# Kernel optimization log

Measured on AMD Instinct MI355X. Metric: run time of the kernel, lower is better.

The kernel has to match this reference:

```python
import jax, jax.numpy as jnp
import numpy as np

B, T, H, NH = 2, 2048, 1024, 16
D = H // NH          # head dim = 64
K_CONV = 4           # short conv kernel size


def _dwconv_silu(x, w):
    # causal depthwise conv1d + silu; x:[B,T,C], w:[C,K]
    Kc = w.shape[1]
    xp = jnp.pad(x, ((0, 0), (Kc - 1, 0), (0, 0))).transpose(0, 2, 1)  # [B,C,T+K-1]
    y = jax.lax.conv_general_dilated(xp, w[:, None, :], (1,), 'VALID',
                                     feature_group_count=w.shape[0],
                                     dimension_numbers=('NCH', 'OIH', 'NCH'))
    return jax.nn.silu(y.transpose(0, 2, 1))


def _l2norm(x, eps=1e-6):
    return x * jax.lax.rsqrt(jnp.sum(x * x, -1, keepdims=True) + eps)


def _forward(hidden, Wq, Wk, Wv, conv_q, conv_k, conv_v, Wb, Wa, A_log, dt_bias, Wg, norm_w, Wo):
    Bh, Tt, Hh = hidden.shape
    nh = A_log.shape[0]
    d = Hh // nh
    q = _dwconv_silu(hidden @ Wq.T, conv_q).reshape(Bh, Tt, nh, d)
    k = _dwconv_silu(hidden @ Wk.T, conv_k).reshape(Bh, Tt, nh, d)
    v = _dwconv_silu(hidden @ Wv.T, conv_v).reshape(Bh, Tt, nh, d)
    q = _l2norm(q) * (d ** -0.5)
    k = _l2norm(k)
    beta = jax.nn.sigmoid(hidden @ Wb.T)                                  # [B,T,h]
    g = -jnp.exp(A_log) * jax.nn.softplus(hidden @ Wa.T + dt_bias)        # [B,T,h]

    def step(S, inp):
        qt, kt, vt, gt, bt = inp
        S = S * jnp.exp(gt)[..., None, None]                 # gated decay
        pred = jnp.einsum('bhk,bhkv->bhv', kt, S)            # current memory readout
        dv = (vt - pred) * bt[..., None]                     # delta-rule update
        S = S + jnp.einsum('bhk,bhv->bhkv', kt, dv)
        ot = jnp.einsum('bhk,bhkv->bhv', qt, S)
        return S, ot

    xs = (q.transpose(1, 0, 2, 3), k.transpose(1, 0, 2, 3), v.transpose(1, 0, 2, 3),
          g.transpose(1, 0, 2), beta.transpose(1, 0, 2))
    S0 = jnp.zeros((Bh, nh, d, d), hidden.dtype)
    _, o = jax.lax.scan(step, S0, xs)
    o = o.transpose(1, 0, 2, 3)                               # [B,T,h,d]
    gate = (hidden @ Wg.T).reshape(Bh, Tt, nh, d)
    o = o * jax.lax.rsqrt(jnp.mean(o * o, -1, keepdims=True) + 1e-5) * norm_w
    o = o * jax.nn.silu(gate)                                 # gated RMSNorm
    return o.reshape(Bh, Tt, Hh) @ Wo.T


def setup_inputs():
    key = jax.random.key(0)
    ks = jax.random.split(key, 16)
    s = 0.02
    return {
        'hidden': jax.random.normal(ks[0], (B, T, H), jnp.float32),
        'Wq': jax.random.normal(ks[1], (H, H), jnp.float32) * s,
        'Wk': jax.random.normal(ks[2], (H, H), jnp.float32) * s,
        'Wv': jax.random.normal(ks[3], (H, H), jnp.float32) * s,
        'conv_q': jax.random.normal(ks[4], (H, K_CONV), jnp.float32) * 0.5,
        'conv_k': jax.random.normal(ks[5], (H, K_CONV), jnp.float32) * 0.5,
        'conv_v': jax.random.normal(ks[6], (H, K_CONV), jnp.float32) * 0.5,
        'Wb': jax.random.normal(ks[7], (NH, H), jnp.float32) * s,
        'Wa': jax.random.normal(ks[8], (NH, H), jnp.float32) * s,
        'A_log': jnp.log(jax.random.uniform(ks[9], (NH,), jnp.float32, 1.0, 16.0)),
        'dt_bias': jnp.log(jnp.expm1(jax.random.uniform(ks[10], (NH,), jnp.float32, 1e-3, 0.1))),
        'Wg': jax.random.normal(ks[11], (H, H), jnp.float32) * s,
        'norm_w': jnp.ones((D,), jnp.float32),
        'Wo': jax.random.normal(ks[12], (H, H), jnp.float32) * s,
    }


def reference(hidden, Wq, Wk, Wv, conv_q, conv_k, conv_v, Wb, Wa, A_log, dt_bias, Wg, norm_w, Wo):
    return _forward(hidden, Wq, Wk, Wv, conv_q, conv_k, conv_v, Wb, Wa, A_log, dt_bias, Wg, norm_w, Wo)
```

## Files before the change

kernel.cpp:

```cpp
#include <hip/hip_runtime.h>
#include <hip/hip_bf16.h>

typedef unsigned short u16;
typedef __attribute__((ext_vector_type(4))) float f32x4;
typedef __attribute__((ext_vector_type(8))) short bf16x8;

#define TLEN 2048
#define NHEAD 16
#define HD 1024

__device__ inline u16 f2bf(float f) {
  unsigned x = __float_as_uint(f);
  return (u16)((x + 0x7fffu + ((x >> 16) & 1u)) >> 16);
}
__device__ inline float bf2f(u16 u) { return __uint_as_float(((unsigned)u) << 16); }

__device__ inline void storev(float* p, float v) { *p = v; }
__device__ inline void storev(u16* p, float v)   { *p = f2bf(v); }

__device__ inline int swz(int row, int col) {
  return (row << 7) + ((((col >> 3) ^ (row & 7)) << 4)) + ((col & 7) << 1);
}
__device__ inline bf16x8 frag(const u16* base, int row, int kslot) {
  return *(const bf16x8*)((const char*)base + (row << 7) +
                          (((kslot ^ (row & 7)) << 4)));
}

__global__ __launch_bounds__(256) void cvt_all(
    const float* __restrict__ h,  const float* __restrict__ wq,
    const float* __restrict__ wk, const float* __restrict__ wv,
    const float* __restrict__ wg, const float* __restrict__ wo,
    const float* __restrict__ Wb, const float* __restrict__ Wa,
    u16* __restrict__ dh,  u16* __restrict__ dhlo,
    u16* __restrict__ dwq, u16* __restrict__ dwk,
    u16* __restrict__ dwv, u16* __restrict__ dwg, u16* __restrict__ dwo,
    u16* __restrict__ dwba_h, u16* __restrict__ dwba_l) {
  const int b = blockIdx.x;
  if (b < 4096) {
    const size_t i = (size_t)b * 256 + threadIdx.x;
    float4 v = *(const float4*)(h + i * 4);
    ushort4 hi, lo;
    hi.x = f2bf(v.x); lo.x = f2bf(v.x - bf2f(hi.x));
    hi.y = f2bf(v.y); lo.y = f2bf(v.y - bf2f(hi.y));
    hi.z = f2bf(v.z); lo.z = f2bf(v.z - bf2f(hi.z));
    hi.w = f2bf(v.w); lo.w = f2bf(v.w - bf2f(hi.w));
    *(ushort4*)(dh + i * 4) = hi;
    *(ushort4*)(dhlo + i * 4) = lo;
  } else if (b < 9216) {
    const int wsel = (b - 4096) >> 10;
    const size_t i = (size_t)((b - 4096) & 1023) * 256 + threadIdx.x;
    const float* s; u16* d;
    switch (wsel) {
      case 0: s = wq; d = dwq; break;
      case 1: s = wk; d = dwk; break;
      case 2: s = wv; d = dwv; break;
      case 3: s = wg; d = dwg; break;
      default: s = wo; d = dwo; break;
    }
    float4 v = *(const float4*)(s + i * 4);
    ushort4 u;
    u.x = f2bf(v.x); u.y = f2bf(v.y); u.z = f2bf(v.z); u.w = f2bf(v.w);
    *(ushort4*)(d + i * 4) = u;
  } else {
    const size_t i = (size_t)(b - 9216) * 256 + threadIdx.x;
    const size_t flat = i * 4;
    const float* src = (flat < 16384) ? (Wb + flat) : (Wa + (flat - 16384));
    float4 v = *(const float4*)src;
    ushort4 hi, lo;
    hi.x = f2bf(v.x); lo.x = f2bf(v.x - bf2f(hi.x));
    hi.y = f2bf(v.y); lo.y = f2bf(v.y - bf2f(hi.y));
    hi.z = f2bf(v.z); lo.z = f2bf(v.z - bf2f(hi.z));
    hi.w = f2bf(v.w); lo.w = f2bf(v.w - bf2f(hi.w));
    *(ushort4*)(dwba_h + flat) = hi;
    *(ushort4*)(dwba_l + flat) = lo;
  }
}

__global__ __launch_bounds__(256, 2) void gemm_big(
    const u16* __restrict__ A,
    const u16* __restrict__ W0p, const u16* __restrict__ W1p,
    const u16* __restrict__ W2p, const u16* __restrict__ W3p,
    u16* __restrict__ C0, u16* __restrict__ C1,
    u16* __restrict__ C2, u16* __restrict__ C3,
    int M, int N, int K) {
  const u16* W; u16* C;
  switch (blockIdx.z) {
    case 0: W = W0p; C = C0; break;
    case 1: W = W1p; C = C1; break;
    case 2: W = W2p; C = C2; break;
    default: W = W3p; C = C3; break;
  }
  const int tid = threadIdx.x;
  const int lane = tid & 63, wid = tid >> 6;
  const int fr = lane & 15, fq = lane >> 4;
  const int row0 = blockIdx.y * 256, col0 = blockIdx.x * 128;
  __shared__ __align__(16) u16 As[256 * 64];
  __shared__ __align__(16) u16 Bs[128 * 64];

  const u16* aSrc[8]; const u16* bSrc[4];
#pragma unroll
  for (int it = 0; it < 8; ++it) {
    const int s = it * 256 + tid;
    const int r = s >> 3, cc = s & 7;
    aSrc[it] = A + (size_t)(row0 + r) * K + (cc ^ (r & 7)) * 8;
  }
#pragma unroll
  for (int it = 0; it < 4; ++it) {
    const int s = it * 256 + tid;
    const int r = s >> 3, cc = s & 7;
    bSrc[it] = W + (size_t)(col0 + r) * K + (cc ^ (r & 7)) * 8;
  }
  int aOff[4][2], bOff[8][2];
#pragma unroll
  for (int m = 0; m < 4; ++m)
#pragma unroll
    for (int kk = 0; kk < 2; ++kk) {
      const int ra = wid * 64 + m * 16 + fr;
      aOff[m][kk] = ra * 128 + ((((kk << 2) | fq) ^ (ra & 7)) << 4);
    }
#pragma unroll
  for (int n = 0; n < 8; ++n)
#pragma unroll
    for (int kk = 0; kk < 2; ++kk) {
      const int rb = n * 16 + fr;
      bOff[n][kk] = rb * 128 + ((((kk << 2) | fq) ^ (rb & 7)) << 4);
    }

  f32x4 acc[4][8] = {};
  for (int k0 = 0; k0 < K; k0 += 64) {
#pragma unroll
    for (int it = 0; it < 8; ++it)
      __builtin_amdgcn_global_load_lds(
          (const __attribute__((address_space(1))) void*)(aSrc[it] + k0),
          (__attribute__((address_space(3))) void*)((char*)As + (it * 256 + tid) * 16),
          16, 0, 0);
#pragma unroll
    for (int it = 0; it < 4; ++it)
      __builtin_amdgcn_global_load_lds(
          (const __attribute__((address_space(1))) void*)(bSrc[it] + k0),
          (__attribute__((address_space(3))) void*)((char*)Bs + (it * 256 + tid) * 16),
          16, 0, 0);
    __syncthreads();
#pragma unroll
    for (int kk = 0; kk < 2; ++kk) {
      bf16x8 af[4], bfr[8];
#pragma unroll
      for (int m = 0; m < 4; ++m)
        af[m] = *(const bf16x8*)((const char*)As + aOff[m][kk]);
#pragma unroll
      for (int n = 0; n < 8; ++n)
        bfr[n] = *(const bf16x8*)((const char*)Bs + bOff[n][kk]);
#pragma unroll
      for (int m = 0; m < 4; ++m)
#pragma unroll
        for (int n = 0; n < 8; ++n)
          acc[m][n] = __builtin_amdgcn_mfma_f32_16x16x32_bf16(af[m], bfr[n], acc[m][n], 0, 0, 0);
    }
    __syncthreads();
  }
#pragma unroll
  for (int m = 0; m < 4; ++m)
#pragma unroll
    for (int n = 0; n < 8; ++n)
#pragma unroll
      for (int r = 0; r < 4; ++r) {
        const int gr = row0 + wid * 64 + m * 16 + fq * 4 + r;
        const int gc = col0 + n * 16 + fr;
        C[(size_t)gr * N + gc] = f2bf(acc[m][n][r]);
      }
}

template <typename OutT, int MT>
__global__ __launch_bounds__(256) void gemm_lin(
    const u16* __restrict__ A, const u16* __restrict__ W,
    OutT* __restrict__ C, int M, int N, int K) {
  const int tid = threadIdx.x;
  const int lane = tid & 63, wid = tid >> 6;
  const int wr = wid >> 1, wc = wid & 1;
  const int fr = lane & 15, fq = lane >> 4;
  const int row0 = blockIdx.y * (MT * 32), col0 = blockIdx.x * 128;
  __shared__ __align__(16) u16 As[MT * 32 * 64];
  __shared__ __align__(16) u16 Bs[128 * 64];

  const u16* aSrc[MT]; const u16* bSrc[4];
#pragma unroll
  for (int it = 0; it < MT; ++it) {
    const int c = it * 256 + tid;
    const int r = c >> 3, cc = c & 7, sc = cc ^ (r & 7);
    aSrc[it] = A + (size_t)(row0 + r) * K + sc * 8;
  }
#pragma unroll
  for (int it = 0; it < 4; ++it) {
    const int c = it * 256 + tid;
    const int r = c >> 3, cc = c & 7, sc = cc ^ (r & 7);
    bSrc[it] = W + (size_t)(col0 + r) * K + sc * 8;
  }
  int aOff[MT][2], bOff[4][2];
#pragma unroll
  for (int m = 0; m < MT; ++m)
#pragma unroll
    for (int kk = 0; kk < 2; ++kk) {
      const int ra = wr * (MT * 16) + m * 16 + fr;
      aOff[m][kk] = ra * 128 + ((((kk << 2) | fq) ^ (fr & 7)) << 4);
    }
#pragma unroll
  for (int n = 0; n < 4; ++n)
#pragma unroll
    for (int kk = 0; kk < 2; ++kk) {
      const int rb = wc * 64 + n * 16 + fr;
      bOff[n][kk] = rb * 128 + ((((kk << 2) | fq) ^ (fr & 7)) << 4);
    }

  f32x4 acc[MT][4] = {};
  for (int k0 = 0; k0 < K; k0 += 64) {
#pragma unroll
    for (int it = 0; it < MT; ++it)
      __builtin_amdgcn_global_load_lds(
          (const __attribute__((address_space(1))) void*)(aSrc[it] + k0),
          (__attribute__((address_space(3))) void*)((char*)As + (it * 256 + wid * 64) * 16),
          16, 0, 0);
#pragma unroll
    for (int it = 0; it < 4; ++it)
      __builtin_amdgcn_global_load_lds(
          (const __attribute__((address_space(1))) void*)(bSrc[it] + k0),
          (__attribute__((address_space(3))) void*)((char*)Bs + (it * 256 + wid * 64) * 16),
          16, 0, 0);
    __syncthreads();
#pragma unroll
    for (int kk = 0; kk < 2; ++kk) {
      bf16x8 af[MT], bfr[4];
#pragma unroll
      for (int m = 0; m < MT; ++m)
        af[m] = *(const bf16x8*)((const char*)As + aOff[m][kk]);
#pragma unroll
      for (int n = 0; n < 4; ++n)
        bfr[n] = *(const bf16x8*)((const char*)Bs + bOff[n][kk]);
#pragma unroll
      for (int m = 0; m < MT; ++m)
#pragma unroll
        for (int n = 0; n < 4; ++n)
          acc[m][n] = __builtin_amdgcn_mfma_f32_16x16x32_bf16(af[m], bfr[n], acc[m][n], 0, 0, 0);
    }
    __syncthreads();
  }
#pragma unroll
  for (int m = 0; m < MT; ++m)
#pragma unroll
    for (int n = 0; n < 4; ++n)
#pragma unroll
      for (int r = 0; r < 4; ++r) {
        const int gr = row0 + wr * (MT * 16) + m * 16 + fq * 4 + r;
        const int gc = col0 + wc * 64 + n * 16 + fr;
        storev(&C[(size_t)gr * N + gc], acc[m][n][r]);
      }
}

__global__ __launch_bounds__(256) void small_mfma(
    const u16* __restrict__ hhi, const u16* __restrict__ hlo,
    const u16* __restrict__ whi, const u16* __restrict__ wlo,
    const float* __restrict__ A_log, const float* __restrict__ dtb,
    float* __restrict__ bbuf, float* __restrict__ gbuf) {
  extern __shared__ char smc[];
  u16* Ahi = (u16*)smc;
  u16* Alo = (u16*)(smc + 32768);
  float* Red = (float*)(smc + 65536);
  const int tid = threadIdx.x;
  const int row0 = blockIdx.x * 16;
#pragma unroll
  for (int i = 0; i < 8; ++i) {
    const int slot = tid + 256 * i;
    const int r = slot >> 7, s = slot & 127;
    const int ss = s ^ (r & 7);
    const size_t src = (size_t)(row0 + r) * 1024 + (size_t)ss * 8;
    __builtin_amdgcn_global_load_lds(
        (const __attribute__((address_space(1))) void*)(hhi + src),
        (__attribute__((address_space(3))) void*)(Ahi + (size_t)slot * 8), 16, 0, 0);
    __builtin_amdgcn_global_load_lds(
        (const __attribute__((address_space(1))) void*)(hlo + src),
        (__attribute__((address_space(3))) void*)(Alo + (size_t)slot * 8), 16, 0, 0);
  }
  __syncthreads();
  const int w = tid >> 6, lane = tid & 63, fr = lane & 15, fq = lane >> 4;
  f32x4 acc[2] = {};
#pragma unroll
  for (int kk = 0; kk < 8; ++kk) {
    const int s = w * 32 + kk * 4 + fq;
    const size_t k = (size_t)w * 256 + kk * 32 + fq * 8;
    const int aoff = ((fr << 7) + (s ^ (fr & 7))) * 8;
    bf16x8 ah = *(const bf16x8*)(Ahi + aoff);
    bf16x8 al = *(const bf16x8*)(Alo + aoff);
#pragma unroll
    for (int ct = 0; ct < 2; ++ct) {
      const size_t boff = (size_t)(ct * 16 + fr) * 1024 + k;
      bf16x8 bh = *(const bf16x8*)(whi + boff);
      bf16x8 bl = *(const bf16x8*)(wlo + boff);
      acc[ct] = __builtin_amdgcn_mfma_f32_16x16x32_bf16(ah, bh, acc[ct], 0, 0, 0);
      acc[ct] = __builtin_amdgcn_mfma_f32_16x16x32_bf16(ah, bl, acc[ct], 0, 0, 0);
      acc[ct] = __builtin_amdgcn_mfma_f32_16x16x32_bf16(al, bh, acc[ct], 0, 0, 0);
    }
  }
#pragma unroll
  for (int ct = 0; ct < 2; ++ct)
#pragma unroll
    for (int rr = 0; rr < 4; ++rr)
      Red[(w * 16 + fq * 4 + rr) * 33 + ct * 16 + fr] = acc[ct][rr];
  __syncthreads();
  if (tid < 128) {
    const int row = tid >> 3, cg = (tid & 7) * 4;
#pragma unroll
    for (int j = 0; j < 4; ++j) {
      const int col = cg + j;
      const float s = Red[(0 * 16 + row) * 33 + col] + Red[(1 * 16 + row) * 33 + col]
                    + Red[(2 * 16 + row) * 33 + col] + Red[(3 * 16 + row) * 33 + col];
      const int grow = row0 + row;
      if (col < 16) {
        bbuf[grow * NHEAD + col] = 1.f / (1.f + __expf(-s));
      } else {
        const int hh = col - 16;
        const float xs = s + dtb[hh];
        const float sp = (xs > 20.f) ? xs : log1pf(__expf(xs));
        gbuf[grow * NHEAD + hh] = -__expf(A_log[hh]) * sp;
      }
    }
  }
}

__global__ __launch_bounds__(256) void chunk_local(
    const u16* __restrict__ qp, const u16* __restrict__ kp, const u16* __restrict__ vp,
    const float* __restrict__ cq, const float* __restrict__ ck, const float* __restrict__ cv,
    const float* __restrict__ gbuf, const float* __restrict__ bbuf,
    u16* __restrict__ Phi, u16* __restrict__ Plo, u16* __restrict__ Ug,
    u16* __restrict__ Rg, u16* __restrict__ Yg) {
  __shared__ __align__(16) u16 Kb[64 * 64];
  __shared__ __align__(16) u16 Qb[64 * 64];
  __shared__ __align__(16) u16 K2T[64 * 64];
  __shared__ __align__(16) u16 KWt[64 * 64];
  __shared__ __align__(16) u16 Vt[64 * 64];
  __shared__ __align__(16) u16 Zb[64 * 64];
  __shared__ __align__(16) u16 Zt[64 * 64];
  __shared__ __align__(16) u16 Mb[64 * 72];
  __shared__ __align__(16) float Cb[16 * 64];
  __shared__ float bcs[64], bet[64], e2v[64], Bv[64];
  u16* WTh = Mb;
  u16* uTh = KWt;
  u16* Gb  = Vt;

  const int bid = blockIdx.x;
  const int c = bid & 31, bh = bid >> 5;
  const int b = bh >> 4, h = bh & 15;
  const int tid = threadIdx.x;

  {
    int* zp = (int*)Zt;
#pragma unroll
    for (int i = 0; i < 8; ++i) zp[tid + 256 * i] = 0;
  }
  if (tid < 64) {
    const size_t gi = (size_t)((b * TLEN + c * 64) + tid) * NHEAD + h;
    bet[tid] = bbuf[gi];
    float v = gbuf[gi];
#pragma unroll
    for (int ofs = 1; ofs < 64; ofs <<= 1) {
      float tt = __shfl_up(v, ofs);
      if (tid >= ofs) v += tt;
    }
    bcs[tid] = v;
  }
  __syncthreads();
  if (tid < 64) {
    const float blast = bcs[63];
    Bv[tid]  = __expf(bcs[tid]);
    e2v[tid] = __expf(blast - bcs[tid]);
  }
  __syncthreads();

  {
    const int dq = (tid & 15) * 4;
    const int col = h * 64 + dq;
    float4 wq4[4], wk4[4], wv4[4];
#pragma unroll
    for (int jj = 0; jj < 4; ++jj) {
      wq4[jj] = *(const float4*)(cq + (size_t)(col + jj) * 4);
      wk4[jj] = *(const float4*)(ck + (size_t)(col + jj) * 4);
      wv4[jj] = *(const float4*)(cv + (size_t)(col + jj) * 4);
    }
#pragma unroll
    for (int i = 0; i < 4; ++i) {
      const int r = i * 16 + (tid >> 4);
      const int tcur = c * 64 + r;
      ushort4 xq[4], xk[4], xv[4];
#pragma unroll
      for (int m = 0; m < 4; ++m) {
        const int tt = tcur - 3 + m;
        if (tt >= 0) {
          const size_t a = (size_t)(b * TLEN + tt) * HD + col;
          xq[m] = *(const ushort4*)(qp + a);
          xk[m] = *(const ushort4*)(kp + a);
          xv[m] = *(const ushort4*)(vp + a);
        } else {
          xq[m] = ushort4{0, 0, 0, 0}; xk[m] = xq[m]; xv[m] = xq[m];
        }
      }
      float yq[4], yk[4], yv[4];
      float ssq = 0.f, ssk = 0.f;
#pragma unroll
      for (int jj = 0; jj < 4; ++jj) {
        float aq = wq4[jj].x * bf2f(((const u16*)&xq[0])[jj]) +
                   wq4[jj].y * bf2f(((const u16*)&xq[1])[jj]) +
                   wq4[jj].z * bf2f(((const u16*)&xq[2])[jj]) +
                   wq4[jj].w * bf2f(((const u16*)&xq[3])[jj]);
        float ak = wk4[jj].x * bf2f(((const u16*)&xk[0])[jj]) +
                   wk4[jj].y * bf2f(((const u16*)&xk[1])[jj]) +
                   wk4[jj].z * bf2f(((const u16*)&xk[2])[jj]) +
                   wk4[jj].w * bf2f(((const u16*)&xk[3])[jj]);
        float av = wv4[jj].x * bf2f(((const u16*)&xv[0])[jj]) +
                   wv4[jj].y * bf2f(((const u16*)&xv[1])[jj]) +
                   wv4[jj].z * bf2f(((const u16*)&xv[2])[jj]) +
                   wv4[jj].w * bf2f(((const u16*)&xv[3])[jj]);
        yq[jj] = aq / (1.f + __expf(-aq));
        yk[jj] = ak / (1.f + __expf(-ak));
        yv[jj] = av / (1.f + __expf(-av));
        ssq += yq[jj] * yq[jj];
        ssk += yk[jj] * yk[jj];
      }
      ssq += __shfl_xor(ssq, 1); ssq += __shfl_xor(ssq, 2);
      ssq += __shfl_xor(ssq, 4); ssq += __shfl_xor(ssq, 8);
      ssk += __shfl_xor(ssk, 1); ssk += __shfl_xor(ssk, 2);
      ssk += __shfl_xor(ssk, 4); ssk += __shfl_xor(ssk, 8);
      const float qsc = rsqrtf(ssq + 1e-6f) * 0.125f;
      const float ksc = rsqrtf(ssk + 1e-6f);
      const float bR = bet[r], e2R = e2v[r], wscR = bR * Bv[r];
      ushort4 qo, ko;
      float kvf[4];
#pragma unroll
      for (int jj = 0; jj < 4; ++jj) kvf[jj] = yk[jj] * ksc;
      qo.x = f2bf(yq[0] * qsc); qo.y = f2bf(yq[1] * qsc);
      qo.z = f2bf(yq[2] * qsc); qo.w = f2bf(yq[3] * qsc);
      ko.x = f2bf(kvf[0]); ko.y = f2bf(kvf[1]);
      ko.z = f2bf(kvf[2]); ko.w = f2bf(kvf[3]);
      *(ushort4*)((char*)Qb + swz(r, dq)) = qo;
      *(ushort4*)((char*)Kb + swz(r, dq)) = ko;
#pragma unroll
      for (int jj = 0; jj < 4; ++jj) {
        *(u16*)((char*)K2T + swz(dq + jj, r)) = f2bf(kvf[jj] * e2R);
        *(u16*)((char*)KWt + swz(dq + jj, r)) = f2bf(kvf[jj] * wscR);
        *(u16*)((char*)Vt  + swz(dq + jj, r)) = f2bf(yv[jj] * bR);
      }
    }
  }
  __syncthreads();

  const int w = tid >> 6, lane = tid & 63, fr = lane & 15, fq = lane >> 4;
  {
    bf16x8 ka0 = frag(Kb, w * 16 + fr, fq);
    bf16x8 ka1 = frag(Kb, w * 16 + fr, 4 + fq);
#pragma unroll
    for (int tc = 0; tc < 4; ++tc) {
      bf16x8 kb0 = frag(Kb, tc * 16 + fr, fq);
      bf16x8 kb1 = frag(Kb, tc * 16 + fr, 4 + fq);
      f32x4 a = {};
      a = __builtin_amdgcn_mfma_f32_16x16x32_bf16(ka0, kb0, a, 0, 0, 0);
      a = __builtin_amdgcn_mfma_f32_16x16x32_bf16(ka1, kb1, a, 0, 0, 0);
#pragma unroll
      for (int rr = 0; rr < 4; ++rr) {
        const int t = w * 16 + fq * 4 + rr, s = tc * 16 + fr;
        const float mv = (s < t) ? bet[t] * __expf(bcs[t] - bcs[s]) * a[rr] : 0.f;
        Mb[t * 72 + s] = f2bf(mv);
      }
    }
  }
  __syncthreads();

#pragma unroll 1
  for (int bi = 0; bi < 4; ++bi) {
    {
      const char* mrow = (const char*)Mb + (size_t)(bi * 16 + fr) * 144;
      bf16x8 ma0 = *(const bf16x8*)(mrow + fq * 16);
      bf16x8 ma1 = *(const bf16x8*)(mrow + 64 + fq * 16);
      bf16x8 zt0 = frag(Zt, w * 16 + fr, fq);
      bf16x8 zt1 = frag(Zt, w * 16 + fr, 4 + fq);
      f32x4 a = {};
      a = __builtin_amdgcn_mfma_f32_16x16x32_bf16(ma0, zt0, a, 0, 0, 0);
      a = __builtin_amdgcn_mfma_f32_16x16x32_bf16(ma1, zt1, a, 0, 0, 0);
#pragma unroll
      for (int rr = 0; rr < 4; ++rr)
        Cb[(fq * 4 + rr) * 64 + w * 16 + fr] = a[rr];
    }
    __syncthreads();
    if (tid < 64) {
      const int j = tid;
      float z[16];
#pragma unroll
      for (int t = 0; t < 16; ++t) {
        float acc = ((bi * 16 + t) == j ? 1.f : 0.f) - Cb[t * 64 + j];
        const u16* mrow = Mb + (size_t)(bi * 16 + t) * 72 + bi * 16;
#pragma unroll
        for (int s = 0; s < t; ++s) acc -= bf2f(mrow[s]) * z[s];
        z[t] = acc;
      }
#pragma unroll
      for (int t = 0; t < 16; ++t)
        *(u16*)((char*)Zb + swz(bi * 16 + t, j)) = f2bf(z[t]);
#pragma unroll
      for (int t4 = 0; t4 < 4; ++t4) {
        ushort4 zz;
        zz.x = f2bf(z[t4 * 4 + 0]); zz.y = f2bf(z[t4 * 4 + 1]);
        zz.z = f2bf(z[t4 * 4 + 2]); zz.w = f2bf(z[t4 * 4 + 3]);
        *(ushort4*)((char*)Zt + swz(j, bi * 16 + t4 * 4)) = zz;
      }
    }
    __syncthreads();
  }

  f32x4 accW[4], accu[4], accG[4];
  {
    bf16x8 kw0 = frag(KWt, w * 16 + fr, fq), kw1 = frag(KWt, w * 16 + fr, 4 + fq);
    bf16x8 vt0 = frag(Vt,  w * 16 + fr, fq), vt1 = frag(Vt,  w * 16 + fr, 4 + fq);
    bf16x8 qa0 = frag(Qb,  w * 16 + fr, fq), qa1 = frag(Qb,  w * 16 + fr, 4 + fq);
#pragma unroll
    for (int tc = 0; tc < 4; ++tc) {
      bf16x8 z0 = frag(Zb, tc * 16 + fr, fq), z1 = frag(Zb, tc * 16 + fr, 4 + fq);
      bf16x8 kb0 = frag(Kb, tc * 16 + fr, fq), kb1 = frag(Kb, tc * 16 + fr, 4 + fq);
      f32x4 aw = {}, au = {}, ag = {};
      aw = __builtin_amdgcn_mfma_f32_16x16x32_bf16(kw0, z0, aw, 0, 0, 0);
      aw = __builtin_amdgcn_mfma_f32_16x16x32_bf16(kw1, z1, aw, 0, 0, 0);
      au = __builtin_amdgcn_mfma_f32_16x16x32_bf16(vt0, z0, au, 0, 0, 0);
      au = __builtin_amdgcn_mfma_f32_16x16x32_bf16(vt1, z1, au, 0, 0, 0);
      ag = __builtin_amdgcn_mfma_f32_16x16x32_bf16(qa0, kb0, ag, 0, 0, 0);
      ag = __builtin_amdgcn_mfma_f32_16x16x32_bf16(qa1, kb1, ag, 0, 0, 0);
      accW[tc] = aw; accu[tc] = au; accG[tc] = ag;
    }
  }
  __syncthreads();
#pragma unroll
  for (int tc = 0; tc < 4; ++tc)
#pragma unroll
    for (int rr = 0; rr < 4; ++rr) {
      const int ro = w * 16 + fq * 4 + rr, co = tc * 16 + fr;
      *(u16*)((char*)WTh + swz(ro, co)) = f2bf(accW[tc][rr]);
      *(u16*)((char*)uTh + swz(ro, co)) = f2bf(accu[tc][rr]);
      const float gv = (co <= ro) ? accG[tc][rr] * __expf(bcs[ro] - bcs[co]) : 0.f;
      *(u16*)((char*)Gb + swz(ro, co)) = f2bf(gv);
    }
  __syncthreads();

  {
    bf16x8 k20 = frag(K2T, w * 16 + fr, fq), k21 = frag(K2T, w * 16 + fr, 4 + fq);
    bf16x8 g0  = frag(Gb,  w * 16 + fr, fq), g1  = frag(Gb,  w * 16 + fr, 4 + fq);
    const float bl = Bv[63];
    const size_t off = (size_t)bid * 4096;
#pragma unroll
    for (int tc = 0; tc < 4; ++tc) {
      bf16x8 w0 = frag(WTh, tc * 16 + fr, fq), w1 = frag(WTh, tc * 16 + fr, 4 + fq);
      bf16x8 u0 = frag(uTh, tc * 16 + fr, fq), u1 = frag(uTh, tc * 16 + fr, 4 + fq);
      f32x4 aP = {}, aU = {}, aR = {}, aY = {};
      aP = __builtin_amdgcn_mfma_f32_16x16x32_bf16(k20, w0, aP, 0, 0, 0);
      aP = __builtin_amdgcn_mfma_f32_16x16x32_bf16(k21, w1, aP, 0, 0, 0);
      aU = __builtin_amdgcn_mfma_f32_16x16x32_bf16(k20, u0, aU, 0, 0, 0);
      aU = __builtin_amdgcn_mfma_f32_16x16x32_bf16(k21, u1, aU, 0, 0, 0);
      aR = __builtin_amdgcn_mfma_f32_16x16x32_bf16(g0, w0, aR, 0, 0, 0);
      aR = __builtin_amdgcn_mfma_f32_16x16x32_bf16(g1, w1, aR, 0, 0, 0);
      aY = __builtin_amdgcn_mfma_f32_16x16x32_bf16(g0, u0, aY, 0, 0, 0);
      aY = __builtin_amdgcn_mfma_f32_16x16x32_bf16(g1, u1, aY, 0, 0, 0);
#pragma unroll
      for (int rr = 0; rr < 4; ++rr) {
        const int ar = w * 16 + fq * 4 + rr, cb = tc * 16 + fr;
        const float pv = ((ar == cb) ? bl : 0.f) - aP[rr];
        const u16 phv = f2bf(pv);
        Phi[off + ar * 64 + cb] = phv;
        Plo[off + ar * 64 + cb] = f2bf(pv - bf2f(phv));
        Ug[off + ar * 64 + cb] = f2bf(aU[rr]);
        const float qv = bf2f(*(const u16*)((const char*)Qb + swz(ar, cb)));
        Rg[off + ar * 64 + cb] = f2bf(Bv[ar] * qv - aR[rr]);
        Yg[off + ar * 64 + cb] = f2bf(aY[rr]);
      }
    }
  }
}

__global__ __launch_bounds__(256) void state_step(
    const u16* __restrict__ Phi, const u16* __restrict__ Plo,
    const u16* __restrict__ Ug, u16* __restrict__ Sst) {
  __shared__ __align__(16) u16 Sth[2][64 * 64];
  __shared__ __align__(16) u16 Stl[2][64 * 64];
  const int bh = blockIdx.x;
  const int tid = threadIdx.x;
  const int w = tid >> 6, lane = tid & 63, fr = lane & 15, fq = lane >> 4;
  const size_t bbase = (size_t)bh * 32 * 4096;
  {
    int* p0 = (int*)&Sth[0][0];
    int* p1 = (int*)&Stl[0][0];
#pragma unroll
    for (int i = 0; i < 8; ++i) { p0[tid + 256 * i] = 0; p1[tid + 256 * i] = 0; }
    const ushort4 z4 = {0, 0, 0, 0};
#pragma unroll
    for (int i = 0; i < 4; ++i)
      *(ushort4*)(Sst + bbase + (size_t)tid * 16 + i * 4) = z4;
  }
  bf16x8 ph[2], pl[2];
  float uin[4][4];
#pragma unroll
  for (int kk = 0; kk < 2; ++kk) {
    const size_t ao = bbase + (size_t)(w * 16 + fr) * 64 + (kk * 4 + fq) * 8;
    ph[kk] = *(const bf16x8*)(Phi + ao);
    pl[kk] = *(const bf16x8*)(Plo + ao);
  }
#pragma unroll
  for (int tc = 0; tc < 4; ++tc)
#pragma unroll
    for (int rr = 0; rr < 4; ++rr)
      uin[tc][rr] = bf2f(Ug[bbase + (size_t)(w * 16 + fq * 4 + rr) * 64 + tc * 16 + fr]);
  __syncthreads();
  int cur = 0;
  for (int c = 0; c < 32; ++c) {
    f32x4 acc[4];
    bf16x8 phc[2] = {ph[0], ph[1]}, plc[2] = {pl[0], pl[1]};
#pragma unroll
    for (int tc = 0; tc < 4; ++tc)
#pragma unroll
      for (int rr = 0; rr < 4; ++rr) acc[tc][rr] = uin[tc][rr];
    if (c + 1 < 32) {
      const size_t off = bbase + (size_t)(c + 1) * 4096;
#pragma unroll
      for (int kk = 0; kk < 2; ++kk) {
        const size_t ao = off + (size_t)(w * 16 + fr) * 64 + (kk * 4 + fq) * 8;
        ph[kk] = *(const bf16x8*)(Phi + ao);
        pl[kk] = *(const bf16x8*)(Plo + ao);
      }
#pragma unroll
      for (int tc = 0; tc < 4; ++tc)
#pragma unroll
        for (int rr = 0; rr < 4; ++rr)
          uin[tc][rr] = bf2f(Ug[off + (size_t)(w * 16 + fq * 4 + rr) * 64 + tc * 16 + fr]);
    }
#pragma unroll
    for (int tc = 0; tc < 4; ++tc) {
#pragma unroll
      for (int kk = 0; kk < 2; ++kk) {
        bf16x8 sh = frag(&Sth[cur][0], tc * 16 + fr, kk * 4 + fq);
        bf16x8 sl = frag(&Stl[cur][0], tc * 16 + fr, kk * 4 + fq);
        acc[tc] = __builtin_amdgcn_mfma_f32_16x16x32_bf16(phc[kk], sh, acc[tc], 0, 0, 0);
        acc[tc] = __builtin_amdgcn_mfma_f32_16x16x32_bf16(phc[kk], sl, acc[tc], 0, 0, 0);
        acc[tc] = __builtin_amdgcn_mfma_f32_16x16x32_bf16(plc[kk], sh, acc[tc], 0, 0, 0);
      }
    }
    const int nxt = cur ^ 1;
    const size_t offn = bbase + (size_t)(c + 1) * 4096;
#pragma unroll
    for (int tc = 0; tc < 4; ++tc)
#pragma unroll
      for (int rr = 0; rr < 4; ++rr) {
        const float v = acc[tc][rr];
        const int row = w * 16 + fq * 4 + rr;
        const int col = tc * 16 + fr;
        const u16 hv = f2bf(v);
        *(u16*)((char*)&Sth[nxt][0] + swz(col, row)) = hv;
        *(u16*)((char*)&Stl[nxt][0] + swz(col, row)) = f2bf(v - bf2f(hv));
        if (c + 1 < 32) Sst[offn + (size_t)row * 64 + col] = hv;
      }
    cur = nxt;
    __syncthreads();
  }
}

__global__ __launch_bounds__(256) void chunk_out(
    const u16* __restrict__ Rg, const u16* __restrict__ Yg,
    const u16* __restrict__ Sst, const u16* __restrict__ gatep,
    const float* __restrict__ norm_w, u16* __restrict__ outb) {
  __shared__ float Rs[64 * 65];
  __shared__ float Ss[64 * 65];
  const int bid = blockIdx.x;
  const int c = bid & 31, bh = bid >> 5, b = bh >> 4, h = bh & 15;
  const int tid = threadIdx.x;
  const size_t off = (size_t)bid * 4096;
#pragma unroll
  for (int i = 0; i < 2; ++i) {
    const int idx = i * 2048 + tid * 8;
    const int row = idx >> 6, col = idx & 63;
    const ushort4 r0 = *(const ushort4*)(Rg + off + idx);
    const ushort4 r1 = *(const ushort4*)(Rg + off + idx + 4);
    const ushort4 s0 = *(const ushort4*)(Sst + off + idx);
    const ushort4 s1 = *(const ushort4*)(Sst + off + idx + 4);
    float* rd = &Rs[row * 65 + col];
    rd[0]=bf2f(r0.x); rd[1]=bf2f(r0.y); rd[2]=bf2f(r0.z); rd[3]=bf2f(r0.w);
    rd[4]=bf2f(r1.x); rd[5]=bf2f(r1.y); rd[6]=bf2f(r1.z); rd[7]=bf2f(r1.w);
    float* sd = &Ss[row * 65 + col];
    sd[0]=bf2f(s0.x); sd[1]=bf2f(s0.y); sd[2]=bf2f(s0.z); sd[3]=bf2f(s0.w);
    sd[4]=bf2f(s1.x); sd[5]=bf2f(s1.y); sd[6]=bf2f(s1.z); sd[7]=bf2f(s1.w);
  }
  __syncthreads();
  const int tr = tid >> 4, tc = tid & 15;
  float acc[4][4];
#pragma unroll
  for (int i = 0; i < 4; ++i) {
    const ushort4 y = *(const ushort4*)(Yg + off + (4*tr+i)*64 + 4*tc);
    acc[i][0] = bf2f(y.x); acc[i][1] = bf2f(y.y);
    acc[i][2] = bf2f(y.z); acc[i][3] = bf2f(y.w);
  }
  for (int k = 0; k < 64; ++k) {
    float r0 = Rs[(4*tr+0)*65+k], r1 = Rs[(4*tr+1)*65+k],
          r2 = Rs[(4*tr+2)*65+k], r3 = Rs[(4*tr+3)*65+k];
    float s0 = Ss[k*65+4*tc+0], s1 = Ss[k*65+4*tc+1],
          s2 = Ss[k*65+4*tc+2], s3 = Ss[k*65+4*tc+3];
    acc[0][0]+=r0*s0; acc[0][1]+=r0*s1; acc[0][2]+=r0*s2; acc[0][3]+=r0*s3;
    acc[1][0]+=r1*s0; acc[1][1]+=r1*s1; acc[1][2]+=r1*s2; acc[1][3]+=r1*s3;
    acc[2][0]+=r2*s0; acc[2][1]+=r2*s1; acc[2][2]+=r2*s2; acc[2][3]+=r2*s3;
    acc[3][0]+=r3*s0; acc[3][1]+=r3*s1; acc[3][2]+=r3*s2; acc[3][3]+=r3*s3;
  }
  const float4 nw4 = *(const float4*)(norm_w + 4 * tc);
  const size_t btbase = (size_t)(b * TLEN + c * 64);
#pragma unroll
  for (int i = 0; i < 4; ++i) {
    float rs = acc[i][0]*acc[i][0] + acc[i][1]*acc[i][1]
             + acc[i][2]*acc[i][2] + acc[i][3]*acc[i][3];
    rs += __shfl_xor(rs, 1); rs += __shfl_xor(rs, 2);
    rs += __shfl_xor(rs, 4); rs += __shfl_xor(rs, 8);
    const float inv = rsqrtf(rs * (1.0f / 64.0f) + 1e-5f);
    const int t = 4 * tr + i;
    const size_t goff = (btbase + t) * 1024 + h * 64 + 4 * tc;
    const ushort4 gv = *(const ushort4*)(gatep + goff);
    const float g0 = bf2f(gv.x), g1 = bf2f(gv.y), g2 = bf2f(gv.z), g3 = bf2f(gv.w);
    ushort4 ov;
    ov.x = f2bf(acc[i][0] * inv * nw4.x * (g0 / (1.f + __expf(-g0))));
    ov.y = f2bf(acc[i][1] * inv * nw4.y * (g1 / (1.f + __expf(-g1))));
    ov.z = f2bf(acc[i][2] * inv * nw4.z * (g2 / (1.f + __expf(-g2))));
    ov.w = f2bf(acc[i][3] * inv * nw4.w * (g3 / (1.f + __expf(-g3))));
    *(ushort4*)(outb + goff) = ov;
  }
}

extern "C" void kernel_launch(void* const* d_in, const int* in_sizes, int n_in,
                              void* d_out, int out_size, void* d_ws, size_t ws_size,
                              hipStream_t stream) {
  const float* hidden = (const float*)d_in[0];
  const float* Wq     = (const float*)d_in[1];
  const float* Wk     = (const float*)d_in[2];
  const float* Wv     = (const float*)d_in[3];
  const float* cq     = (const float*)d_in[4];
  const float* ck     = (const float*)d_in[5];
  const float* cv     = (const float*)d_in[6];
  const float* Wb     = (const float*)d_in[7];
  const float* Wa     = (const float*)d_in[8];
  const float* A_log  = (const float*)d_in[9];
  const float* dtb    = (const float*)d_in[10];
  const float* Wg     = (const float*)d_in[11];
  const float* nw     = (const float*)d_in[12];
  const float* Wo     = (const float*)d_in[13];

  char* p = (char*)d_ws;
  const size_t MB = 1u << 20;
  u16* h_bf = (u16*)(p + 0 * MB);
  u16* wq_b = (u16*)(p + 8 * MB);
  u16* wk_b = (u16*)(p + 10 * MB);
  u16* wv_b = (u16*)(p + 12 * MB);
  u16* wg_b = (u16*)(p + 14 * MB);
  u16* Phi = (u16*)(p + 0 * MB);
  u16* Plo = (u16*)(p + 8 * MB);
  u16* wo_b = (u16*)(p + 16 * MB);
  u16* qp_b = (u16*)(p + 18 * MB);
  u16* kp_b = (u16*)(p + 26 * MB);
  u16* vp_b = (u16*)(p + 34 * MB);
  u16* gp_b = (u16*)(p + 42 * MB);
  u16*   of_b = vp_b;
  float* gbuf = (float*)(p + 50 * MB);
  float* bbuf = (float*)(p + 50 * MB + 262144);
  u16* Ug  = (u16*)(p + 51 * MB);
  u16* Rg  = (u16*)(p + 59 * MB);
  u16* Yg  = (u16*)(p + 67 * MB);
  u16* Sst = (u16*)(p + 75 * MB);
  u16* hlo_b = (u16*)(p + 83 * MB);
  u16* wba_h = (u16*)(p + 91 * MB);
  u16* wba_l = (u16*)(p + 91 * MB + 65536);

  cvt_all<<<9248, 256, 0, stream>>>(hidden, Wq, Wk, Wv, Wg, Wo, Wb, Wa,
                                    h_bf, hlo_b, wq_b, wk_b, wv_b, wg_b, wo_b,
                                    wba_h, wba_l);

  gemm_big<<<dim3(8, 16, 4), 256, 0, stream>>>(
      h_bf, wq_b, wk_b, wv_b, wg_b, qp_b, kp_b, vp_b, gp_b, 4096, 1024, 1024);

  const int sm_lds = 65536 + 8448;
  hipFuncSetAttribute((const void*)small_mfma,
                      hipFuncAttributeMaxDynamicSharedMemorySize, sm_lds);
  small_mfma<<<256, 256, sm_lds, stream>>>(h_bf, hlo_b, wba_h, wba_l,
                                           A_log, dtb, bbuf, gbuf);

  chunk_local<<<1024, 256, 0, stream>>>(qp_b, kp_b, vp_b, cq, ck, cv,
                                        gbuf, bbuf, Phi, Plo, Ug, Rg, Yg);
  state_step<<<32, 256, 0, stream>>>(Phi, Plo, Ug, Sst);
  chunk_out<<<1024, 256, 0, stream>>>(Rg, Yg, Sst, gp_b, nw, of_b);

  gemm_lin<float, 2><<<dim3(8, 64, 1), 256, 0, stream>>>(
      of_b, wo_b, (float*)d_out, 4096, 1024, 1024);
}
```

Baseline: 181.4 us.

## Use MFMA in chunk_out, packed bf16 conversions, and a revised LDS swizzle

Several unrelated changes. chunk_out drops its fp32 LDS FMA loop and instead runs bf16 MFMA straight from global memory, reading a transposed stored state that the scan kernel now writes with vector stores. Float-to-bf16 rounding throughout now uses the packed v_cvt_pk_bf16_f32 instruction. The LDS swizzle XOR pattern now mixes in higher row bits to cut bank conflicts. The rounding path changes from the manual routine to the hardware conversion, which may differ slightly on NaN or edge values.

```diff
diff --git a/kernel.cpp b/kernel.cpp
--- a/kernel.cpp
+++ b/kernel.cpp
@@ -15,15 +15,22 @@
 }
 __device__ inline float bf2f(u16 u) { return __uint_as_float(((unsigned)u) << 16); }
 
+__device__ inline unsigned pkbf(float lo, float hi) {
+  unsigned r;
+  asm("v_cvt_pk_bf16_f32 %0, %1, %2" : "=v"(r) : "v"(lo), "v"(hi));
+  return r;
+}
+
 __device__ inline void storev(float* p, float v) { *p = v; }
 __device__ inline void storev(u16* p, float v)   { *p = f2bf(v); }
 
+__device__ inline int rowx(int row) { return (row ^ (row >> 3)) & 7; }
 __device__ inline int swz(int row, int col) {
-  return (row << 7) + ((((col >> 3) ^ (row & 7)) << 4)) + ((col & 7) << 1);
+  return (row << 7) + (((col >> 3) ^ rowx(row)) << 4) + ((col & 7) << 1);
 }
 __device__ inline bf16x8 frag(const u16* base, int row, int kslot) {
   return *(const bf16x8*)((const char*)base + (row << 7) +
-                          (((kslot ^ (row & 7)) << 4)));
+                          ((kslot ^ rowx(row)) << 4));
 }
 
 __global__ __launch_bounds__(256) void cvt_all(
@@ -161,13 +168,16 @@
 #pragma unroll
   for (int m = 0; m < 4; ++m)
 #pragma unroll
-    for (int n = 0; n < 8; ++n)
-#pragma unroll
-      for (int r = 0; r < 4; ++r) {
-        const int gr = row0 + wid * 64 + m * 16 + fq * 4 + r;
-        const int gc = col0 + n * 16 + fr;
-        C[(size_t)gr * N + gc] = f2bf(acc[m][n][r]);
-      }
+    for (int n = 0; n < 8; ++n) {
+      const int gr0 = row0 + wid * 64 + m * 16 + fq * 4;
+      const int gc = col0 + n * 16 + fr;
+      const unsigned c01 = pkbf(acc[m][n][0], acc[m][n][1]);
+      const unsigned c23 = pkbf(acc[m][n][2], acc[m][n][3]);
+      C[(size_t)(gr0 + 0) * N + gc] = (u16)c01;
+      C[(size_t)(gr0 + 1) * N + gc] = (u16)(c01 >> 16);
+      C[(size_t)(gr0 + 2) * N + gc] = (u16)c23;
+      C[(size_t)(gr0 + 3) * N + gc] = (u16)(c23 >> 16);
+    }
 }
 
 template <typename OutT, int MT>
@@ -430,27 +440,40 @@
       const float qsc = rsqrtf(ssq + 1e-6f) * 0.125f;
       const float ksc = rsqrtf(ssk + 1e-6f);
       const float bR = bet[r], e2R = e2v[r], wscR = bR * Bv[r];
-      ushort4 qo, ko;
       float kvf[4];
 #pragma unroll
       for (int jj = 0; jj < 4; ++jj) kvf[jj] = yk[jj] * ksc;
-      qo.x = f2bf(yq[0] * qsc); qo.y = f2bf(yq[1] * qsc);
-      qo.z = f2bf(yq[2] * qsc); qo.w = f2bf(yq[3] * qsc);
-      ko.x = f2bf(kvf[0]); ko.y = f2bf(kvf[1]);
-      ko.z = f2bf(kvf[2]); ko.w = f2bf(kvf[3]);
-      *(ushort4*)((char*)Qb + swz(r, dq)) = qo;
-      *(ushort4*)((char*)Kb + swz(r, dq)) = ko;
-#pragma unroll
-      for (int jj = 0; jj < 4; ++jj) {
-        *(u16*)((char*)K2T + swz(dq + jj, r)) = f2bf(kvf[jj] * e2R);
-        *(u16*)((char*)KWt + swz(dq + jj, r)) = f2bf(kvf[jj] * wscR);
-        *(u16*)((char*)Vt  + swz(dq + jj, r)) = f2bf(yv[jj] * bR);
-      }
+      uint2 qo2, ko2;
+      qo2.x = pkbf(yq[0] * qsc, yq[1] * qsc);
+      qo2.y = pkbf(yq[2] * qsc, yq[3] * qsc);
+      ko2.x = pkbf(kvf[0], kvf[1]);
+      ko2.y = pkbf(kvf[2], kvf[3]);
+      *(uint2*)((char*)Qb + swz(r, dq)) = qo2;
+      *(uint2*)((char*)Kb + swz(r, dq)) = ko2;
+      const unsigned k2a = pkbf(kvf[0] * e2R, kvf[1] * e2R);
+      const unsigned k2b = pkbf(kvf[2] * e2R, kvf[3] * e2R);
+      const unsigned kwa = pkbf(kvf[0] * wscR, kvf[1] * wscR);
+      const unsigned kwb = pkbf(kvf[2] * wscR, kvf[3] * wscR);
+      const unsigned vta = pkbf(yv[0] * bR, yv[1] * bR);
+      const unsigned vtb = pkbf(yv[2] * bR, yv[3] * bR);
+      *(u16*)((char*)K2T + swz(dq + 0, r)) = (u16)k2a;
+      *(u16*)((char*)K2T + swz(dq + 1, r)) = (u16)(k2a >> 16);
+      *(u16*)((char*)K2T + swz(dq + 2, r)) = (u16)k2b;
+      *(u16*)((char*)K2T + swz(dq + 3, r)) = (u16)(k2b >> 16);
+      *(u16*)((char*)KWt + swz(dq + 0, r)) = (u16)kwa;
+      *(u16*)((char*)KWt + swz(dq + 1, r)) = (u16)(kwa >> 16);
+      *(u16*)((char*)KWt + swz(dq + 2, r)) = (u16)kwb;
+      *(u16*)((char*)KWt + swz(dq + 3, r)) = (u16)(kwb >> 16);
+      *(u16*)((char*)Vt + swz(dq + 0, r)) = (u16)vta;
+      *(u16*)((char*)Vt + swz(dq + 1, r)) = (u16)(vta >> 16);
+      *(u16*)((char*)Vt + swz(dq + 2, r)) = (u16)vtb;
+      *(u16*)((char*)Vt + swz(dq + 3, r)) = (u16)(vtb >> 16);
     }
   }
   __syncthreads();
 
   const int w = tid >> 6, lane = tid & 63, fr = lane & 15, fq = lane >> 4;
+  const int t0r = w * 16 + fq * 4;
   {
     bf16x8 ka0 = frag(Kb, w * 16 + fr, fq);
     bf16x8 ka1 = frag(Kb, w * 16 + fr, 4 + fq);
@@ -461,12 +484,18 @@
       f32x4 a = {};
       a = __builtin_amdgcn_mfma_f32_16x16x32_bf16(ka0, kb0, a, 0, 0, 0);
       a = __builtin_amdgcn_mfma_f32_16x16x32_bf16(ka1, kb1, a, 0, 0, 0);
+      const int s = tc * 16 + fr;
+      float mv[4];
 #pragma unroll
       for (int rr = 0; rr < 4; ++rr) {
-        const int t = w * 16 + fq * 4 + rr, s = tc * 16 + fr;
-        const float mv = (s < t) ? bet[t] * __expf(bcs[t] - bcs[s]) * a[rr] : 0.f;
-        Mb[t * 72 + s] = f2bf(mv);
-      }
+        const int t = t0r + rr;
+        mv[rr] = (s < t) ? bet[t] * __expf(bcs[t] - bcs[s]) * a[rr] : 0.f;
+      }
+      const unsigned m01 = pkbf(mv[0], mv[1]), m23 = pkbf(mv[2], mv[3]);
+      Mb[(t0r + 0) * 72 + s] = (u16)m01;
+      Mb[(t0r + 1) * 72 + s] = (u16)(m01 >> 16);
+      Mb[(t0r + 2) * 72 + s] = (u16)m23;
+      Mb[(t0r + 3) * 72 + s] = (u16)(m23 >> 16);
     }
   }
   __syncthreads();
@@ -498,15 +527,18 @@
         for (int s = 0; s < t; ++s) acc -= bf2f(mrow[s]) * z[s];
         z[t] = acc;
       }
-#pragma unroll
-      for (int t = 0; t < 16; ++t)
-        *(u16*)((char*)Zb + swz(bi * 16 + t, j)) = f2bf(z[t]);
+      unsigned zw[8];
+#pragma unroll
+      for (int t2 = 0; t2 < 8; ++t2) zw[t2] = pkbf(z[2 * t2], z[2 * t2 + 1]);
+#pragma unroll
+      for (int t2 = 0; t2 < 8; ++t2) {
+        *(u16*)((char*)Zb + swz(bi * 16 + 2 * t2, j)) = (u16)zw[t2];
+        *(u16*)((char*)Zb + swz(bi * 16 + 2 * t2 + 1, j)) = (u16)(zw[t2] >> 16);
+      }
 #pragma unroll
       for (int t4 = 0; t4 < 4; ++t4) {
-        ushort4 zz;
-        zz.x = f2bf(z[t4 * 4 + 0]); zz.y = f2bf(z[t4 * 4 + 1]);
-        zz.z = f2bf(z[t4 * 4 + 2]); zz.w = f2bf(z[t4 * 4 + 3]);
-        *(ushort4*)((char*)Zt + swz(j, bi * 16 + t4 * 4)) = zz;
+        uint2 zz; zz.x = zw[2 * t4]; zz.y = zw[2 * t4 + 1];
+        *(uint2*)((char*)Zt + swz(j, bi * 16 + t4 * 4)) = zz;
       }
     }
     __syncthreads();
@@ -533,15 +565,32 @@
   }
   __syncthreads();
 #pragma unroll
-  for (int tc = 0; tc < 4; ++tc)
+  for (int tc = 0; tc < 4; ++tc) {
+    const int co = tc * 16 + fr;
+    const unsigned w01 = pkbf(accW[tc][0], accW[tc][1]);
+    const unsigned w23 = pkbf(accW[tc][2], accW[tc][3]);
+    const unsigned u01 = pkbf(accu[tc][0], accu[tc][1]);
+    const unsigned u23 = pkbf(accu[tc][2], accu[tc][3]);
+    float gv[4];
 #pragma unroll
     for (int rr = 0; rr < 4; ++rr) {
-      const int ro = w * 16 + fq * 4 + rr, co = tc * 16 + fr;
-      *(u16*)((char*)WTh + swz(ro, co)) = f2bf(accW[tc][rr]);
-      *(u16*)((char*)uTh + swz(ro, co)) = f2bf(accu[tc][rr]);
-      const float gv = (co <= ro) ? accG[tc][rr] * __expf(bcs[ro] - bcs[co]) : 0.f;
-      *(u16*)((char*)Gb + swz(ro, co)) = f2bf(gv);
-    }
+      const int ro = t0r + rr;
+      gv[rr] = (co <= ro) ? accG[tc][rr] * __expf(bcs[ro] - bcs[co]) : 0.f;
+    }
+    const unsigned g01 = pkbf(gv[0], gv[1]), g23 = pkbf(gv[2], gv[3]);
+    *(u16*)((char*)WTh + swz(t0r + 0, co)) = (u16)w01;
+    *(u16*)((char*)WTh + swz(t0r + 1, co)) = (u16)(w01 >> 16);
+    *(u16*)((char*)WTh + swz(t0r + 2, co)) = (u16)w23;
+    *(u16*)((char*)WTh + swz(t0r + 3, co)) = (u16)(w23 >> 16);
+    *(u16*)((char*)uTh + swz(t0r + 0, co)) = (u16)u01;
+    *(u16*)((char*)uTh + swz(t0r + 1, co)) = (u16)(u01 >> 16);
+    *(u16*)((char*)uTh + swz(t0r + 2, co)) = (u16)u23;
+    *(u16*)((char*)uTh + swz(t0r + 3, co)) = (u16)(u23 >> 16);
+    *(u16*)((char*)Gb + swz(t0r + 0, co)) = (u16)g01;
+    *(u16*)((char*)Gb + swz(t0r + 1, co)) = (u16)(g01 >> 16);
+    *(u16*)((char*)Gb + swz(t0r + 2, co)) = (u16)g23;
+    *(u16*)((char*)Gb + swz(t0r + 3, co)) = (u16)(g23 >> 16);
+  }
   __syncthreads();
 
   {
@@ -562,18 +611,36 @@
       aR = __builtin_amdgcn_mfma_f32_16x16x32_bf16(g1, w1, aR, 0, 0, 0);
       aY = __builtin_amdgcn_mfma_f32_16x16x32_bf16(g0, u0, aY, 0, 0, 0);
       aY = __builtin_amdgcn_mfma_f32_16x16x32_bf16(g1, u1, aY, 0, 0, 0);
+      const int cb = tc * 16 + fr;
+      float pv[4], rv[4];
 #pragma unroll
       for (int rr = 0; rr < 4; ++rr) {
-        const int ar = w * 16 + fq * 4 + rr, cb = tc * 16 + fr;
-        const float pv = ((ar == cb) ? bl : 0.f) - aP[rr];
-        const u16 phv = f2bf(pv);
-        Phi[off + ar * 64 + cb] = phv;
-        Plo[off + ar * 64 + cb] = f2bf(pv - bf2f(phv));
-        Ug[off + ar * 64 + cb] = f2bf(aU[rr]);
+        const int ar = t0r + rr;
+        pv[rr] = ((ar == cb) ? bl : 0.f) - aP[rr];
         const float qv = bf2f(*(const u16*)((const char*)Qb + swz(ar, cb)));
-        Rg[off + ar * 64 + cb] = f2bf(Bv[ar] * qv - aR[rr]);
-        Yg[off + ar * 64 + cb] = f2bf(aY[rr]);
-      }
+        rv[rr] = Bv[ar] * qv - aR[rr];
+      }
+      const unsigned p01 = pkbf(pv[0], pv[1]), p23 = pkbf(pv[2], pv[3]);
+      const float l0 = pv[0] - bf2f((u16)p01), l1 = pv[1] - bf2f((u16)(p01 >> 16));
+      const float l2 = pv[2] - bf2f((u16)p23), l3 = pv[3] - bf2f((u16)(p23 >> 16));
+      const unsigned q01 = pkbf(l0, l1), q23 = pkbf(l2, l3);
+      const unsigned u01 = pkbf(aU[0], aU[1]), u23 = pkbf(aU[2], aU[3]);
+      const unsigned r01 = pkbf(rv[0], rv[1]), r23 = pkbf(rv[2], rv[3]);
+      const unsigned y01 = pkbf(aY[0], aY[1]), y23 = pkbf(aY[2], aY[3]);
+      const size_t o0 = off + (size_t)(t0r + 0) * 64 + cb;
+      const size_t o1 = off + (size_t)(t0r + 1) * 64 + cb;
+      const size_t o2 = off + (size_t)(t0r + 2) * 64 + cb;
+      const size_t o3 = off + (size_t)(t0r + 3) * 64 + cb;
+      Phi[o0] = (u16)p01; Phi[o1] = (u16)(p01 >> 16);
+      Phi[o2] = (u16)p23; Phi[o3] = (u16)(p23 >> 16);
+      Plo[o0] = (u16)q01; Plo[o1] = (u16)(q01 >> 16);
+      Plo[o2] = (u16)q23; Plo[o3] = (u16)(q23 >> 16);
+      Ug[o0] = (u16)u01; Ug[o1] = (u16)(u01 >> 16);
+      Ug[o2] = (u16)u23; Ug[o3] = (u16)(u23 >> 16);
+      Rg[o0] = (u16)r01; Rg[o1] = (u16)(r01 >> 16);
+      Rg[o2] = (u16)r23; Rg[o3] = (u16)(r23 >> 16);
+      Yg[o0] = (u16)y01; Yg[o1] = (u16)(y01 >> 16);
+      Yg[o2] = (u16)y23; Yg[o3] = (u16)(y23 >> 16);
     }
   }
 }
@@ -586,6 +653,7 @@
   const int bh = blockIdx.x;
   const int tid = threadIdx.x;
   const int w = tid >> 6, lane = tid & 63, fr = lane & 15, fq = lane >> 4;
+  const int ar0 = w * 16 + fq * 4;
   const size_t bbase = (size_t)bh * 32 * 4096;
   {
     int* p0 = (int*)&Sth[0][0];
@@ -609,7 +677,7 @@
   for (int tc = 0; tc < 4; ++tc)
 #pragma unroll
     for (int rr = 0; rr < 4; ++rr)
-      uin[tc][rr] = bf2f(Ug[bbase + (size_t)(w * 16 + fq * 4 + rr) * 64 + tc * 16 + fr]);
+      uin[tc][rr] = bf2f(Ug[bbase + (size_t)(ar0 + rr) * 64 + tc * 16 + fr]);
   __syncthreads();
   int cur = 0;
   for (int c = 0; c < 32; ++c) {
@@ -631,7 +699,7 @@
       for (int tc = 0; tc < 4; ++tc)
 #pragma unroll
         for (int rr = 0; rr < 4; ++rr)
-          uin[tc][rr] = bf2f(Ug[off + (size_t)(w * 16 + fq * 4 + rr) * 64 + tc * 16 + fr]);
+          uin[tc][rr] = bf2f(Ug[off + (size_t)(ar0 + rr) * 64 + tc * 16 + fr]);
     }
 #pragma unroll
     for (int tc = 0; tc < 4; ++tc) {
@@ -647,17 +715,21 @@
     const int nxt = cur ^ 1;
     const size_t offn = bbase + (size_t)(c + 1) * 4096;
 #pragma unroll
-    for (int tc = 0; tc < 4; ++tc)
-#pragma unroll
-      for (int rr = 0; rr < 4; ++rr) {
-        const float v = acc[tc][rr];
-        const int row = w * 16 + fq * 4 + rr;
-        const int col = tc * 16 + fr;
-        const u16 hv = f2bf(v);
-        *(u16*)((char*)&Sth[nxt][0] + swz(col, row)) = hv;
-        *(u16*)((char*)&Stl[nxt][0] + swz(col, row)) = f2bf(v - bf2f(hv));
-        if (c + 1 < 32) Sst[offn + (size_t)row * 64 + col] = hv;
-      }
+    for (int tc = 0; tc < 4; ++tc) {
+      const int col = tc * 16 + fr;
+      const unsigned h01 = pkbf(acc[tc][0], acc[tc][1]);
+      const unsigned h23 = pkbf(acc[tc][2], acc[tc][3]);
+      const float l0 = acc[tc][0] - bf2f((u16)h01);
+      const float l1 = acc[tc][1] - bf2f((u16)(h01 >> 16));
+      const float l2 = acc[tc][2] - bf2f((u16)h23);
+      const float l3 = acc[tc][3] - bf2f((u16)(h23 >> 16));
+      uint2 hh; hh.x = h01; hh.y = h23;
+      uint2 ll; ll.x = pkbf(l0, l1); ll.y = pkbf(l2, l3);
+      *(uint2*)((char*)&Sth[nxt][0] + swz(col, ar0)) = hh;
+      *(uint2*)((char*)&Stl[nxt][0] + swz(col, ar0)) = ll;
+      if (c + 1 < 32)
+        *(uint2*)(Sst + offn + (size_t)col * 64 + ar0) = hh;
+    }
     cur = nxt;
     __syncthreads();
   }
@@ -665,67 +737,51 @@
 
 __global__ __launch_bounds__(256) void chunk_out(
     const u16* __restrict__ Rg, const u16* __restrict__ Yg,
-    const u16* __restrict__ Sst, const u16* __restrict__ gatep,
+    const u16* __restrict__ SstT, const u16* __restrict__ gatep,
     const float* __restrict__ norm_w, u16* __restrict__ outb) {
-  __shared__ float Rs[64 * 65];
-  __shared__ float Ss[64 * 65];
   const int bid = blockIdx.x;
   const int c = bid & 31, bh = bid >> 5, b = bh >> 4, h = bh & 15;
   const int tid = threadIdx.x;
+  const int w = tid >> 6, lane = tid & 63, fr = lane & 15, fq = lane >> 4;
+  const int ar0 = w * 16 + fq * 4;
   const size_t off = (size_t)bid * 4096;
-#pragma unroll
-  for (int i = 0; i < 2; ++i) {
-    const int idx = i * 2048 + tid * 8;
-    const int row = idx >> 6, col = idx & 63;
-    const ushort4 r0 = *(const ushort4*)(Rg + off + idx);
-    const ushort4 r1 = *(const ushort4*)(Rg + off + idx + 4);
-    const ushort4 s0 = *(const ushort4*)(Sst + off + idx);
-    const ushort4 s1 = *(const ushort4*)(Sst + off + idx + 4);
-    float* rd = &Rs[row * 65 + col];
-    rd[0]=bf2f(r0.x); rd[1]=bf2f(r0.y); rd[2]=bf2f(r0.z); rd[3]=bf2f(r0.w);
-    rd[4]=bf2f(r1.x); rd[5]=bf2f(r1.y); rd[6]=bf2f(r1.z); rd[7]=bf2f(r1.w);
-    float* sd = &Ss[row * 65 + col];
-    sd[0]=bf2f(s0.x); sd[1]=bf2f(s0.y); sd[2]=bf2f(s0.z); sd[3]=bf2f(s0.w);
-    sd[4]=bf2f(s1.x); sd[5]=bf2f(s1.y); sd[6]=bf2f(s1.z); sd[7]=bf2f(s1.w);
-  }
-  __syncthreads();
-  const int tr = tid >> 4, tc = tid & 15;
-  float acc[4][4];
-#pragma unroll
-  for (int i = 0; i < 4; ++i) {
-    const ushort4 y = *(const ushort4*)(Yg + off + (4*tr+i)*64 + 4*tc);
-    acc[i][0] = bf2f(y.x); acc[i][1] = bf2f(y.y);
-    acc[i][2] = bf2f(y.z); acc[i][3] = bf2f(y.w);
-  }
-  for (int k = 0; k < 64; ++k) {
-    float r0 = Rs[(4*tr+0)*65+k], r1 = Rs[(4*tr+1)*65+k],
-          r2 = Rs[(4*tr+2)*65+k], r3 = Rs[(4*tr+3)*65+k];
-    float s0 = Ss[k*65+4*tc+0], s1 = Ss[k*65+4*tc+1],
-          s2 = Ss[k*65+4*tc+2], s3 = Ss[k*65+4*tc+3];
-    acc[0][0]+=r0*s0; acc[0][1]+=r0*s1; acc[0][2]+=r0*s2; acc[0][3]+=r0*s3;
-    acc[1][0]+=r1*s0; acc[1][1]+=r1*s1; acc[1][2]+=r1*s2; acc[1][3]+=r1*s3;
-    acc[2][0]+=r2*s0; acc[2][1]+=r2*s1; acc[2][2]+=r2*s2; acc[2][3]+=r2*s3;
-    acc[3][0]+=r3*s0; acc[3][1]+=r3*s1; acc[3][2]+=r3*s2; acc[3][3]+=r3*s3;
-  }
-  const float4 nw4 = *(const float4*)(norm_w + 4 * tc);
+  bf16x8 ra[2];
+#pragma unroll
+  for (int kk = 0; kk < 2; ++kk)
+    ra[kk] = *(const bf16x8*)(Rg + off + (size_t)(w * 16 + fr) * 64 + (kk * 4 + fq) * 8);
+  f32x4 acc[4];
+#pragma unroll
+  for (int tc = 0; tc < 4; ++tc)
+#pragma unroll
+    for (int rr = 0; rr < 4; ++rr)
+      acc[tc][rr] = bf2f(Yg[off + (size_t)(ar0 + rr) * 64 + tc * 16 + fr]);
+#pragma unroll
+  for (int tc = 0; tc < 4; ++tc)
+#pragma unroll
+    for (int kk = 0; kk < 2; ++kk) {
+      bf16x8 sb = *(const bf16x8*)(SstT + off + (size_t)(tc * 16 + fr) * 64 + (kk * 4 + fq) * 8);
+      acc[tc] = __builtin_amdgcn_mfma_f32_16x16x32_bf16(ra[kk], sb, acc[tc], 0, 0, 0);
+    }
+  float nwv[4];
+#pragma unroll
+  for (int tc = 0; tc < 4; ++tc) nwv[tc] = norm_w[tc * 16 + fr];
   const size_t btbase = (size_t)(b * TLEN + c * 64);
 #pragma unroll
-  for (int i = 0; i < 4; ++i) {
-    float rs = acc[i][0]*acc[i][0] + acc[i][1]*acc[i][1]
-             + acc[i][2]*acc[i][2] + acc[i][3]*acc[i][3];
+  for (int rr = 0; rr < 4; ++rr) {
+    const int t = ar0 + rr;
+    float rs = acc[0][rr] * acc[0][rr] + acc[1][rr] * acc[1][rr]
+             + acc[2][rr] * acc[2][rr] + acc[3][rr] * acc[3][rr];
     rs += __shfl_xor(rs, 1); rs += __shfl_xor(rs, 2);
     rs += __shfl_xor(rs, 4); rs += __shfl_xor(rs, 8);
     const float inv = rsqrtf(rs * (1.0f / 64.0f) + 1e-5f);
-    const int t = 4 * tr + i;
-    const size_t goff = (btbase + t) * 1024 + h * 64 + 4 * tc;
-    const ushort4 gv = *(const ushort4*)(gatep + goff);
-    const float g0 = bf2f(gv.x), g1 = bf2f(gv.y), g2 = bf2f(gv.z), g3 = bf2f(gv.w);
-    ushort4 ov;
-    ov.x = f2bf(acc[i][0] * inv * nw4.x * (g0 / (1.f + __expf(-g0))));
-    ov.y = f2bf(acc[i][1] * inv * nw4.y * (g1 / (1.f + __expf(-g1))));
-    ov.z = f2bf(acc[i][2] * inv * nw4.z * (g2 / (1.f + __expf(-g2))));
-    ov.w = f2bf(acc[i][3] * inv * nw4.w * (g3 / (1.f + __expf(-g3))));
-    *(ushort4*)(outb + goff) = ov;
+    const size_t rowoff = (btbase + t) * 1024 + h * 64;
+#pragma unroll
+    for (int tc = 0; tc < 4; ++tc) {
+      const int j = tc * 16 + fr;
+      const float g = bf2f(gatep[rowoff + j]);
+      const float val = acc[tc][rr] * inv * nwv[tc] * (g / (1.f + __expf(-g)));
+      outb[rowoff + j] = f2bf(val);
+    }
   }
 }
 
```

Result: faster. 170.5 us (-6.0%).
